# Performance work log

Measured on AMD Instinct MI355X. Metric: run time of the kernel, lower is better.

The kernel has to match this reference:

```python
import jax, jax.numpy as jnp
import numpy as np

TEMPERATURE = 0.07
NORM_EPS = 1e-12   # F.normalize eps
LOG_EPS = 1e-08


def setup_inputs() -> dict:
    key = jax.random.key(0)
    k1, k2 = jax.random.split(key)
    N, D, C = 8192, 512, 64
    projections = jax.random.normal(k1, (N, D), dtype=jnp.float32)
    targets = jax.random.randint(k2, (N,), 0, C, dtype=jnp.int64)
    return {"projections": projections, "targets": targets}


def reference(projections, targets):
    # L2-normalize rows (matches F.normalize: x / max(||x||, eps))
    norm = jnp.linalg.norm(projections, axis=1, keepdims=True)
    p = projections / jnp.maximum(norm, NORM_EPS)

    # [N, N] cosine similarity / temperature
    sim = jnp.matmul(p, p.T) / TEMPERATURE
    # row-max subtraction for numerical stability (gradient flows through max,
    # as in the torch original)
    sim = sim - jnp.max(sim, axis=1, keepdims=True)
    exp_sim = jnp.exp(sim)

    n = projections.shape[0]
    eye = jnp.eye(n, dtype=bool)
    mask_self = ~eye                                   # exclude self-pairs
    mask_pos = (targets[:, None] == targets[None, :]) & mask_self

    denom = jnp.sum(jnp.where(mask_self, exp_sim, 0.0), axis=1, keepdims=True)
    log_prob = sim - jnp.log(denom + LOG_EPS)

    num = jnp.sum(jnp.where(mask_pos, log_prob, 0.0), axis=1)
    cnt = jnp.sum(mask_pos, axis=1).astype(log_prob.dtype)
    # divide_no_nan: 0 where cnt == 0
    loss_per_sample = jnp.where(cnt == 0, 0.0, num / jnp.where(cnt == 0, 1.0, cnt))
    return loss_per_sample
```

## Files before the change

kernel.cpp:

```cpp
#include <hip/hip_runtime.h>
#include <hip/hip_bf16.h>
#include <math.h>

#define N_ROWS 8192
#define DIM    512
#define NCLS   64
#define BM     256
#define BK     64
#define NKT    (DIM / BK)
#define NTILE  (N_ROWS / BM)
#define NTRI   (NTILE * (NTILE + 1) / 2)
#define NSLOT  NTILE
#define M_CONST 14.285714285714286f
#define L2E     1.4426950408889634f
#define M2_CONST 20.60992915555662f
#define SCALE2  4.539815541256959f

using bf16x8 = __attribute__((ext_vector_type(8))) short;
using f32x4  = __attribute__((ext_vector_type(4))) float;

static __device__ inline unsigned short f2bf(float x) {
  unsigned u = __float_as_uint(x);
  unsigned r = u + 0x7FFFu + ((u >> 16) & 1u);
  return (unsigned short)(r >> 16);
}

__global__ __launch_bounds__(256) void normalize_rows(const float* __restrict__ proj,
                                                      unsigned short* __restrict__ outb) {
  const int row  = blockIdx.x * 4 + (threadIdx.x >> 6);
  const int lane = threadIdx.x & 63;
  const float4* src = (const float4*)(proj + (size_t)row * DIM);
  float4 a = src[lane * 2];
  float4 b = src[lane * 2 + 1];
  float ss = a.x*a.x + a.y*a.y + a.z*a.z + a.w*a.w
           + b.x*b.x + b.y*b.y + b.z*b.z + b.w*b.w;
#pragma unroll
  for (int off = 1; off < 64; off <<= 1) ss += __shfl_xor(ss, off);
  const float scale = SCALE2 / fmaxf(sqrtf(ss), 1e-12f);
  float v[8] = {a.x, a.y, a.z, a.w, b.x, b.y, b.z, b.w};
  unsigned short h[8];
#pragma unroll
  for (int i = 0; i < 8; ++i) h[i] = f2bf(v[i] * scale);
  uint4 packed;
  packed.x = (unsigned)h[0] | ((unsigned)h[1] << 16);
  packed.y = (unsigned)h[2] | ((unsigned)h[3] << 16);
  packed.z = (unsigned)h[4] | ((unsigned)h[5] << 16);
  packed.w = (unsigned)h[6] | ((unsigned)h[7] << 16);
  *(uint4*)(outb + (size_t)row * DIM + lane * 8) = packed;
}

__attribute__((amdgpu_waves_per_eu(4, 4)))
__global__ __launch_bounds__(1024) void supcon_tile(const unsigned short* __restrict__ p16,
                                                    const int* __restrict__ tgt,
                                                    float* __restrict__ dpart,
                                                    float* __restrict__ spart) {
  const int logical = ((int)blockIdx.x & 7) * (NTRI / 8) + ((int)blockIdx.x >> 3);
  int rem = logical, br = 0;
  while (rem >= NTILE - br) { rem -= NTILE - br; ++br; }
  const int bc = br + rem;

  __shared__ short As[2][BM * BK];
  __shared__ short Bs[2][BM * BK];
  __shared__ int   tgr[BM], tgc[BM];
  __shared__ float redE[4][BM], redS[4][BM];
  __shared__ float redEc[4][BM], redSc[4][BM];

  const int tid  = threadIdx.x;
  const int lane = tid & 63;
  const int wid  = tid >> 6;
  const int wm = wid >> 2, wn = wid & 3;
  const int lhi = lane >> 4, llo = lane & 15;
  const int swz = llo & 7;

  const int aoff = (wm * 64 + llo) * BK;
  const int boff = (wn * 64 + llo) * BK;
  const int kc0  = ((lhi) ^ swz) * 8;
  const int kc1  = ((4 + lhi) ^ swz) * 8;

  const size_t rowA0 = (size_t)br * BM;
  const size_t rowB0 = (size_t)bc * BM;

#define STAGE(BUF, KT) do {                                                         \
  _Pragma("unroll")                                                                 \
  for (int j = 0; j < 2; ++j) {                                                     \
    const int g  = tid + j * 1024;                                                  \
    const int r  = g >> 3, gp = g & 7;                                              \
    const int gl = gp ^ (r & 7);                                                    \
    const unsigned short* sA = p16 + (rowA0 + r) * DIM + (KT) * BK + gl * 8;        \
    const unsigned short* sB = p16 + (rowB0 + r) * DIM + (KT) * BK + gl * 8;        \
    __builtin_amdgcn_global_load_lds((const __attribute__((address_space(1))) void*)sA, \
        (__attribute__((address_space(3))) void*)&As[BUF][g * 8], 16, 0, 0);        \
    __builtin_amdgcn_global_load_lds((const __attribute__((address_space(1))) void*)sB, \
        (__attribute__((address_space(3))) void*)&Bs[BUF][g * 8], 16, 0, 0);        \
  }                                                                                 \
} while (0)

  STAGE(0, 0);
  if (tid < BM)            tgr[tid] = tgt[br * BM + tid];
  else if (tid < 2 * BM)   tgc[tid - BM] = tgt[bc * BM + (tid - BM)];

  f32x4 zero = {0.f, 0.f, 0.f, 0.f};
  f32x4 acc[4][4];
#pragma unroll
  for (int i = 0; i < 4; ++i)
#pragma unroll
    for (int j = 0; j < 4; ++j) acc[i][j] = zero;

  __syncthreads();

#pragma unroll
  for (int kt = 0; kt < NKT; ++kt) {
    const int cur = kt & 1, nxt = cur ^ 1;

    if (kt > 0) {
      __builtin_amdgcn_s_barrier();
      __builtin_amdgcn_sched_barrier(0);
    }
    if (kt + 1 < NKT) {
      STAGE(nxt, kt + 1);
      asm volatile("s_waitcnt vmcnt(4)" ::: "memory");
    } else {
      asm volatile("s_waitcnt vmcnt(0)" ::: "memory");
    }
    __builtin_amdgcn_sched_barrier(0);
    __builtin_amdgcn_s_barrier();
    __builtin_amdgcn_sched_barrier(0);

    const short* As_c = &As[cur][aoff];
    const short* Bs_c = &Bs[cur][boff];
#pragma unroll
    for (int ks = 0; ks < 2; ++ks) {
      const int kc = ks ? kc1 : kc0;
      bf16x8 af[4], bfr[4];
#pragma unroll
      for (int mi = 0; mi < 4; ++mi)
        af[mi] = *(const bf16x8*)(As_c + kc + mi * (16 * BK));
#pragma unroll
      for (int ni = 0; ni < 4; ++ni)
        bfr[ni] = *(const bf16x8*)(Bs_c + kc + ni * (16 * BK));
#pragma unroll
      for (int mi = 0; mi < 4; ++mi)
#pragma unroll
        for (int ni = 0; ni < 4; ++ni)
          acc[mi][ni] = __builtin_amdgcn_mfma_f32_16x16x32_bf16(af[mi], bfr[ni], acc[mi][ni], 0, 0, 0);
    }
  }
#undef STAGE

  const bool diag = (br == bc);
  int tc[4];
#pragma unroll
  for (int ni = 0; ni < 4; ++ni) tc[ni] = tgc[wn * 64 + ni * 16 + llo];
  float ecol[4] = {0.f, 0.f, 0.f, 0.f};
  float scol[4] = {0.f, 0.f, 0.f, 0.f};

#pragma unroll
  for (int mi = 0; mi < 4; ++mi) {
#pragma unroll
    for (int rg = 0; rg < 4; ++rg) {
      const int rin  = wm * 64 + mi * 16 + lhi * 4 + rg;
      const int trow = tgr[rin];
      float esum = 0.f, ssum = 0.f;
#pragma unroll
      for (int ni = 0; ni < 4; ++ni) {
        const int cin = wn * 64 + ni * 16 + llo;
        const float x = acc[mi][ni][rg];
        const bool self = diag && (rin == cin);
        const float e = self ? 0.f : __builtin_amdgcn_exp2f(x - M2_CONST);
        const bool pos = (!self) && (trow == tc[ni]);
        const float sv = pos ? x : 0.f;
        esum += e;  ssum += sv;
        ecol[ni] += e;  scol[ni] += sv;
      }
#pragma unroll
      for (int off = 1; off < 16; off <<= 1) {
        esum += __shfl_xor(esum, off);
        ssum += __shfl_xor(ssum, off);
      }
      if (llo == 0) { redE[wn][rin] = esum; redS[wn][rin] = ssum; }
    }
  }
  if (!diag) {
#pragma unroll
    for (int ni = 0; ni < 4; ++ni) {
      float ec = ecol[ni], sc = scol[ni];
      ec += __shfl_xor(ec, 16); ec += __shfl_xor(ec, 32);
      sc += __shfl_xor(sc, 16); sc += __shfl_xor(sc, 32);
      if (lhi == 0) {
        redEc[wm][wn * 64 + ni * 16 + llo] = ec;
        redSc[wm][wn * 64 + ni * 16 + llo] = sc;
      }
    }
  }
  __syncthreads();

  if (tid < BM) {
    const float e = redE[0][tid] + redE[1][tid] + redE[2][tid] + redE[3][tid];
    const float s = redS[0][tid] + redS[1][tid] + redS[2][tid] + redS[3][tid];
    dpart[(size_t)bc * N_ROWS + rowA0 + tid] = e;
    spart[(size_t)bc * N_ROWS + rowA0 + tid] = s;
  } else if (tid < 2 * BM && !diag) {
    const int c = tid - BM;
    dpart[(size_t)br * N_ROWS + rowB0 + c] = redEc[0][c] + redEc[1][c] + redEc[2][c] + redEc[3][c];
    spart[(size_t)br * N_ROWS + rowB0 + c] = redSc[0][c] + redSc[1][c] + redSc[2][c] + redSc[3][c];
  }
}

__global__ __launch_bounds__(256) void combine_loss(const float* __restrict__ dpart,
                                                    const float* __restrict__ spart,
                                                    const int* __restrict__ tgt,
                                                    float* __restrict__ out) {
  __shared__ float dsh[4][64], ssh[4][64];
  __shared__ int   hloc[NCLS];
  const int tid  = threadIdx.x;
  const int lane = tid & 63;
  const int g    = tid >> 6;
  const int r    = blockIdx.x * 64 + lane;

  if (tid < NCLS) hloc[tid] = 0;
  __syncthreads();
  for (int i = tid; i < N_ROWS; i += 256) atomicAdd(&hloc[tgt[i]], 1);

  float d = 0.f, s = 0.f;
  for (int k = g * (NSLOT / 4); k < (g + 1) * (NSLOT / 4); ++k) {
    d += dpart[(size_t)k * N_ROWS + r];
    s += spart[(size_t)k * N_ROWS + r];
  }
  dsh[g][lane] = d; ssh[g][lane] = s;
  __syncthreads();
  if (g == 0) {
    d = dsh[0][lane] + dsh[1][lane] + dsh[2][lane] + dsh[3][lane];
    s = ssh[0][lane] + ssh[1][lane] + ssh[2][lane] + ssh[3][lane];
    const int cnt = hloc[tgt[r]] - 1;
    out[r] = (cnt > 0) ? (s / (L2E * (float)cnt) - M_CONST - logf(d + 1e-8f)) : 0.f;
  }
}

extern "C" void kernel_launch(void* const* d_in, const int* in_sizes, int n_in,
                              void* d_out, int out_size, void* d_ws, size_t ws_size,
                              hipStream_t stream) {
  const float* proj = (const float*)d_in[0];
  const int*   tgt  = (const int*)d_in[1];
  float* out = (float*)d_out;

  char* ws = (char*)d_ws;
  unsigned short* p16  = (unsigned short*)ws;
  float* dpart = (float*)(ws + (size_t)8 * 1024 * 1024);
  float* spart = (float*)(ws + (size_t)9 * 1024 * 1024);

  normalize_rows<<<N_ROWS / 4, 256, 0, stream>>>(proj, p16);
  supcon_tile<<<NTRI, 1024, 0, stream>>>(p16, tgt, dpart, spart);
  combine_loss<<<N_ROWS / 64, 256, 0, stream>>>(dpart, spart, tgt, out);
}
```

Baseline: 96.65 us.

## Switch symmetric tiling to 256x128 rectangular tiles with strict-upper masking

```diff
diff --git a/kernel.cpp b/kernel.cpp
--- a/kernel.cpp
+++ b/kernel.cpp
@@ -5,12 +5,14 @@
 #define N_ROWS 8192
 #define DIM    512
 #define NCLS   64
-#define BM     256
+#define BMR    256
+#define BNC    128
 #define BK     64
 #define NKT    (DIM / BK)
-#define NTILE  (N_ROWS / BM)
-#define NTRI   (NTILE * (NTILE + 1) / 2)
-#define NSLOT  NTILE
+#define NRT    (N_ROWS / BMR)
+#define NCT    (N_ROWS / BNC)
+#define NBLK   1056
+#define NSLOT  (NCT + NRT)
 #define M_CONST 14.285714285714286f
 #define L2E     1.4426950408889634f
 #define M2_CONST 20.60992915555662f
@@ -49,55 +51,60 @@
   *(uint4*)(outb + (size_t)row * DIM + lane * 8) = packed;
 }
 
-__attribute__((amdgpu_waves_per_eu(4, 4)))
-__global__ __launch_bounds__(1024) void supcon_tile(const unsigned short* __restrict__ p16,
-                                                    const int* __restrict__ tgt,
-                                                    float* __restrict__ dpart,
-                                                    float* __restrict__ spart) {
-  const int logical = ((int)blockIdx.x & 7) * (NTRI / 8) + ((int)blockIdx.x >> 3);
-  int rem = logical, br = 0;
-  while (rem >= NTILE - br) { rem -= NTILE - br; ++br; }
-  const int bc = br + rem;
-
-  __shared__ short As[2][BM * BK];
-  __shared__ short Bs[2][BM * BK];
-  __shared__ int   tgr[BM], tgc[BM];
-  __shared__ float redE[4][BM], redS[4][BM];
-  __shared__ float redEc[4][BM], redSc[4][BM];
+__global__ __launch_bounds__(512) void supcon_tile(const unsigned short* __restrict__ p16,
+                                                   const int* __restrict__ tgt,
+                                                   float* __restrict__ dpart,
+                                                   float* __restrict__ spart) {
+  const int logical = ((int)blockIdx.x & 7) * (NBLK / 8) + ((int)blockIdx.x >> 3);
+  int rem = logical, bi = 0;
+  while (rem >= NCT - 2 * bi) { rem -= NCT - 2 * bi; ++bi; }
+  const int bj = 2 * bi + rem;
+
+  __shared__ short As[2][BMR * BK];
+  __shared__ short Bs[2][BNC * BK];
+  __shared__ int   tgr[BMR], tgc[BNC];
+  __shared__ float redE[2][BMR], redS[2][BMR];
+  __shared__ float redEc[4][BNC], redSc[4][BNC];
 
   const int tid  = threadIdx.x;
   const int lane = tid & 63;
   const int wid  = tid >> 6;
-  const int wm = wid >> 2, wn = wid & 3;
+  const int wm = wid >> 1, wn = wid & 1;
   const int lhi = lane >> 4, llo = lane & 15;
   const int swz = llo & 7;
 
+  const size_t rowA0 = (size_t)bi * BMR;
+  const size_t colB0 = (size_t)bj * BNC;
+
   const int aoff = (wm * 64 + llo) * BK;
   const int boff = (wn * 64 + llo) * BK;
-  const int kc0  = ((lhi) ^ swz) * 8;
+  const int kc0  = (lhi ^ swz) * 8;
   const int kc1  = ((4 + lhi) ^ swz) * 8;
-
-  const size_t rowA0 = (size_t)br * BM;
-  const size_t rowB0 = (size_t)bc * BM;
 
 #define STAGE(BUF, KT) do {                                                         \
   _Pragma("unroll")                                                                 \
-  for (int j = 0; j < 2; ++j) {                                                     \
-    const int g  = tid + j * 1024;                                                  \
+  for (int j = 0; j < 4; ++j) {                                                     \
+    const int g  = tid + j * 512;                                                   \
     const int r  = g >> 3, gp = g & 7;                                              \
     const int gl = gp ^ (r & 7);                                                    \
     const unsigned short* sA = p16 + (rowA0 + r) * DIM + (KT) * BK + gl * 8;        \
-    const unsigned short* sB = p16 + (rowB0 + r) * DIM + (KT) * BK + gl * 8;        \
     __builtin_amdgcn_global_load_lds((const __attribute__((address_space(1))) void*)sA, \
         (__attribute__((address_space(3))) void*)&As[BUF][g * 8], 16, 0, 0);        \
+  }                                                                                 \
+  _Pragma("unroll")                                                                 \
+  for (int j = 0; j < 2; ++j) {                                                     \
+    const int g  = tid + j * 512;                                                   \
+    const int r  = g >> 3, gp = g & 7;                                              \
+    const int gl = gp ^ (r & 7);                                                    \
+    const unsigned short* sB = p16 + (colB0 + r) * DIM + (KT) * BK + gl * 8;        \
     __builtin_amdgcn_global_load_lds((const __attribute__((address_space(1))) void*)sB, \
         (__attribute__((address_space(3))) void*)&Bs[BUF][g * 8], 16, 0, 0);        \
   }                                                                                 \
 } while (0)
 
   STAGE(0, 0);
-  if (tid < BM)            tgr[tid] = tgt[br * BM + tid];
-  else if (tid < 2 * BM)   tgc[tid - BM] = tgt[bc * BM + (tid - BM)];
+  if (tid < BMR)                 tgr[tid] = tgt[rowA0 + tid];
+  else if (tid < BMR + BNC)      tgc[tid - BMR] = tgt[colB0 + (tid - BMR)];
 
   f32x4 zero = {0.f, 0.f, 0.f, 0.f};
   f32x4 acc[4][4];
@@ -118,7 +125,7 @@
     }
     if (kt + 1 < NKT) {
       STAGE(nxt, kt + 1);
-      asm volatile("s_waitcnt vmcnt(4)" ::: "memory");
+      asm volatile("s_waitcnt vmcnt(6)" ::: "memory");
     } else {
       asm volatile("s_waitcnt vmcnt(0)" ::: "memory");
     }
@@ -147,7 +154,6 @@
   }
 #undef STAGE
 
-  const bool diag = (br == bc);
   int tc[4];
 #pragma unroll
   for (int ni = 0; ni < 4; ++ni) tc[ni] = tgc[wn * 64 + ni * 16 + llo];
@@ -159,15 +165,17 @@
 #pragma unroll
     for (int rg = 0; rg < 4; ++rg) {
       const int rin  = wm * 64 + mi * 16 + lhi * 4 + rg;
+      const int rg_g = (int)rowA0 + rin;
       const int trow = tgr[rin];
       float esum = 0.f, ssum = 0.f;
 #pragma unroll
       for (int ni = 0; ni < 4; ++ni) {
-        const int cin = wn * 64 + ni * 16 + llo;
+        const int cin  = wn * 64 + ni * 16 + llo;
+        const int cg_g = (int)colB0 + cin;
         const float x = acc[mi][ni][rg];
-        const bool self = diag && (rin == cin);
-        const float e = self ? 0.f : __builtin_amdgcn_exp2f(x - M2_CONST);
-        const bool pos = (!self) && (trow == tc[ni]);
+        const bool valid = cg_g > rg_g;
+        const float e = valid ? __builtin_amdgcn_exp2f(x - M2_CONST) : 0.f;
+        const bool pos = valid && (trow == tc[ni]);
         const float sv = pos ? x : 0.f;
         esum += e;  ssum += sv;
         ecol[ni] += e;  scol[ni] += sv;
@@ -180,29 +188,27 @@
       if (llo == 0) { redE[wn][rin] = esum; redS[wn][rin] = ssum; }
     }
   }
-  if (!diag) {
-#pragma unroll
-    for (int ni = 0; ni < 4; ++ni) {
-      float ec = ecol[ni], sc = scol[ni];
-      ec += __shfl_xor(ec, 16); ec += __shfl_xor(ec, 32);
-      sc += __shfl_xor(sc, 16); sc += __shfl_xor(sc, 32);
-      if (lhi == 0) {
-        redEc[wm][wn * 64 + ni * 16 + llo] = ec;
-        redSc[wm][wn * 64 + ni * 16 + llo] = sc;
-      }
-    }
-  }
-  __syncthreads();
-
-  if (tid < BM) {
-    const float e = redE[0][tid] + redE[1][tid] + redE[2][tid] + redE[3][tid];
-    const float s = redS[0][tid] + redS[1][tid] + redS[2][tid] + redS[3][tid];
-    dpart[(size_t)bc * N_ROWS + rowA0 + tid] = e;
-    spart[(size_t)bc * N_ROWS + rowA0 + tid] = s;
-  } else if (tid < 2 * BM && !diag) {
-    const int c = tid - BM;
-    dpart[(size_t)br * N_ROWS + rowB0 + c] = redEc[0][c] + redEc[1][c] + redEc[2][c] + redEc[3][c];
-    spart[(size_t)br * N_ROWS + rowB0 + c] = redSc[0][c] + redSc[1][c] + redSc[2][c] + redSc[3][c];
+#pragma unroll
+  for (int ni = 0; ni < 4; ++ni) {
+    float ec = ecol[ni], sc = scol[ni];
+    ec += __shfl_xor(ec, 16); ec += __shfl_xor(ec, 32);
+    sc += __shfl_xor(sc, 16); sc += __shfl_xor(sc, 32);
+    if (lhi == 0) {
+      redEc[wm][wn * 64 + ni * 16 + llo] = ec;
+      redSc[wm][wn * 64 + ni * 16 + llo] = sc;
+    }
+  }
+  __syncthreads();
+
+  if (tid < BMR) {
+    dpart[(size_t)bj * N_ROWS + rowA0 + tid] = redE[0][tid] + redE[1][tid];
+    spart[(size_t)bj * N_ROWS + rowA0 + tid] = redS[0][tid] + redS[1][tid];
+  } else if (tid < BMR + BNC) {
+    const int c = tid - BMR;
+    dpart[(size_t)(NCT + bi) * N_ROWS + colB0 + c] =
+        redEc[0][c] + redEc[1][c] + redEc[2][c] + redEc[3][c];
+    spart[(size_t)(NCT + bi) * N_ROWS + colB0 + c] =
+        redSc[0][c] + redSc[1][c] + redSc[2][c] + redSc[3][c];
   }
 }
 
@@ -246,9 +252,10 @@
   char* ws = (char*)d_ws;
   unsigned short* p16  = (unsigned short*)ws;
   float* dpart = (float*)(ws + (size_t)8 * 1024 * 1024);
-  float* spart = (float*)(ws + (size_t)9 * 1024 * 1024);
-
+  float* spart = (float*)(ws + (size_t)11 * 1024 * 1024);
+
+  (void)hipMemsetAsync(dpart, 0, (size_t)2 * NSLOT * N_ROWS * sizeof(float), stream);
   normalize_rows<<<N_ROWS / 4, 256, 0, stream>>>(proj, p16);
-  supcon_tile<<<NTRI, 1024, 0, stream>>>(p16, tgt, dpart, spart);
+  supcon_tile<<<NBLK, 512, 0, stream>>>(p16, tgt, dpart, spart);
   combine_loss<<<N_ROWS / 64, 256, 0, stream>>>(dpart, spart, tgt, out);
 }
```

After: 99.26 us. 2.7% more time.
